# Optimization experiments

Hardware: AMD Instinct MI355X
Metric: run time of the kernel (lower is better)

Reference implementation:

```python
import jax, jax.numpy as jnp
import numpy as np

N = 100000   # nodes
E = 800000   # edges
H = 4        # heads
C = 32       # out_channels (== in_channels)
IN = 32      # in_channels
ED = 16      # edge_dim
RBF_IN = 42  # sbf_dim*6 (input to lin_rbf)
SBF_IN = 16  # rbf_dim (input to lin_sbf)


def _glorot(key, shape):
    fan_in = shape[0]
    return jax.random.normal(key, shape, dtype=jnp.float32) / np.sqrt(fan_in).astype(np.float32)


def setup_inputs() -> dict:
    key = jax.random.key(0)
    ks = jax.random.split(key, 20)
    inp = {
        "x": jax.random.normal(ks[0], (N, IN), dtype=jnp.float32),
        "edge_attr": jax.random.normal(ks[1], (E, ED), dtype=jnp.float32),
        "rbf": jax.random.normal(ks[2], (N, RBF_IN), dtype=jnp.float32),
        "sbf": jax.random.normal(ks[3], (E, H, SBF_IN), dtype=jnp.float32),
        # params (weights stored [in, out] for y = x @ W)
        "w_rbf0": _glorot(ks[4], (RBF_IN, IN)),
        "w_rbf1": _glorot(ks[5], (IN, IN)),
        "w_sbf0": _glorot(ks[6], (SBF_IN, IN)),
        "w_sbf1": _glorot(ks[7], (IN, IN)),
        "w_ek": _glorot(ks[8], (ED, H * C)),
        "w_ev": _glorot(ks[9], (ED, H * C)),
        "w_k": _glorot(ks[10], (IN, H * C)),
        "b_k": jnp.zeros((H * C,), dtype=jnp.float32),
        "w_q": _glorot(ks[11], (IN, H * C)),
        "b_q": jnp.zeros((H * C,), dtype=jnp.float32),
        "w_v": _glorot(ks[12], (IN, H * C)),
        "b_v": jnp.zeros((H * C,), dtype=jnp.float32),
        "w_skip": _glorot(ks[13], (IN, H * C)),
        "b_skip": jnp.zeros((H * C,), dtype=jnp.float32),
        "edge_index": jax.random.randint(ks[14], (2, E), 0, N, dtype=jnp.int32),
        "edge_index_0": jax.random.randint(ks[15], (E,), 0, N, dtype=jnp.int32),  # unused by forward
    }
    return inp


def reference(x, edge_attr, rbf, sbf,
              w_rbf0, w_rbf1, w_sbf0, w_sbf1,
              w_ek, w_ev, w_k, b_k, w_q, b_q, w_v, b_v,
              w_skip, b_skip, edge_index, edge_index_0):
    src, dst = edge_index[0], edge_index[1]
    # filters (source swaps rbf/sbf naming; we follow forward() exactly)
    rbf_filter = (rbf @ w_rbf0) @ w_rbf1            # [N, IN]
    sbf_filter = (sbf @ w_sbf0) @ w_sbf1            # [E, H, C]

    x_src = rbf_filter * x                          # [N, IN]
    key = (x_src @ w_k + b_k).reshape(-1, H, C)     # [N, H, C]
    query = (x @ w_q + b_q).reshape(-1, H, C)
    value = (x_src @ w_v + b_v).reshape(-1, H, C)

    edge_key = (edge_attr @ w_ek).reshape(-1, H, C)  # [E, H, C]
    edge_val = (edge_attr @ w_ev).reshape(-1, H, C)

    key_j = key[src] + edge_key                     # gather + add [E, H, C]
    value_j = value[src] + edge_val
    query_i = query[dst]

    inv_sqrt_c = np.float32(1.0 / np.sqrt(C))
    alpha = (query_i * key_j).sum(axis=-1) * inv_sqrt_c   # [E, H]

    # segment softmax over destination nodes
    amax = jax.ops.segment_max(alpha, dst, num_segments=N)
    amax = jnp.where(jnp.isfinite(amax), amax, 0.0)
    ex = jnp.exp(alpha - amax[dst])
    denom = jax.ops.segment_sum(ex, dst, num_segments=N)
    alpha = ex / (denom[dst] + np.float32(1e-16))         # [E, H]

    # dropout p=0.0 -> identity
    message = value_j * alpha[:, :, None] * sbf_filter    # [E, H, C]
    aggr = jax.ops.segment_sum(message, dst, num_segments=N)  # [N, H, C]

    out = aggr.reshape(N, H * C) + (x @ w_skip + b_skip)  # concat + root skip
    return out
```

## Files before the change

kernel.cpp:

```cpp
#include <hip/hip_runtime.h>
#include <hip/hip_bf16.h>

#define NN 100000
#define EE 800000
#define SLOT 64

typedef unsigned short u16;

__device__ __forceinline__ float bf2f(u16 u){ return __uint_as_float(((unsigned)u)<<16); }
__device__ __forceinline__ u16 f2bf(float f){
  unsigned u = __float_as_uint(f);
  u += 0x7fffu + ((u>>16)&1u);
  return (u16)(u>>16);
}
__device__ __forceinline__ float lo16(unsigned v){ return __uint_as_float(v<<16); }
__device__ __forceinline__ float hi16(unsigned v){ return __uint_as_float(v & 0xffff0000u); }

__device__ __forceinline__ void cvt8(uint4 u, float* f){
  f[0]=lo16(u.x); f[1]=hi16(u.x);
  f[2]=lo16(u.y); f[3]=hi16(u.y);
  f[4]=lo16(u.z); f[5]=hi16(u.z);
  f[6]=lo16(u.w); f[7]=hi16(u.w);
}

__global__ void kprep(const float* w_rbf0, const float* w_rbf1, const float* w_sbf0, const float* w_sbf1,
                      const float* w_k, const float* b_k, const float* w_q, const float* b_q,
                      const float* w_v, const float* b_v, const float* w_skip, const float* b_skip,
                      float* Wrbfc, float* Wsbfc,
                      float2* wkv, float2* wqs, float2* bkv, float2* bqs)
{
  int b = blockIdx.x;
  if (b==0){
    for (int idx=threadIdx.x; idx<42*32; idx+=blockDim.x){
      int k=idx>>5, c=idx&31;
      float acc=0.f;
      for (int j=0;j<32;j++) acc += w_rbf0[k*32+j]*w_rbf1[j*32+c];
      Wrbfc[idx]=acc;
    }
  } else if (b==1){
    for (int idx=threadIdx.x; idx<16*32; idx+=blockDim.x){
      int k=idx>>5, c=idx&31;
      float acc=0.f;
      for (int j=0;j<32;j++) acc += w_sbf0[k*32+j]*w_sbf1[j*32+c];
      Wsbfc[idx]=acc;
    }
  } else if (b==2){
    for (int idx=threadIdx.x; idx<4096; idx+=blockDim.x){
      wkv[idx]=make_float2(w_k[idx], w_v[idx]);
      wqs[idx]=make_float2(w_q[idx], w_skip[idx]);
    }
  } else {
    for (int idx=threadIdx.x; idx<128; idx+=blockDim.x){
      bkv[idx]=make_float2(b_k[idx], b_v[idx]);
      bqs[idx]=make_float2(b_q[idx], b_skip[idx]);
    }
  }
}

__global__ void kscatter(const int* ei, int* cnt, int* slots){
  int e = blockIdx.x*blockDim.x + threadIdx.x;
  if (e < EE){
    int dst = ei[EE+e];
    int pos = atomicAdd(&cnt[dst], 1);
    if (pos < SLOT) slots[(long)dst*SLOT+pos] = e;
  }
}

__global__ void __launch_bounds__(256) knode(const float* x, const float* rbf, const float* Wrbfc,
                                             const float2* wkv_g, const float2* wqs_g,
                                             const float2* bkv_g, const float2* bqs_g,
                                             u16* key, u16* value, u16* query, float* outp)
{
  __shared__ float2 wkv[4096];
  __shared__ float2 wqs[4096];
  __shared__ float  Wr[42*32];
  __shared__ float2 bkv[128], bqs[128];
  __shared__ float  xs[2][32], xsrcs[2][32], rbfs[2][42];
  for (int i=threadIdx.x;i<4096;i+=256){ wkv[i]=wkv_g[i]; wqs[i]=wqs_g[i]; }
  for (int i=threadIdx.x;i<1344;i+=256) Wr[i]=Wrbfc[i];
  if (threadIdx.x<128){ bkv[threadIdx.x]=bkv_g[threadIdx.x]; bqs[threadIdx.x]=bqs_g[threadIdx.x]; }
  __syncthreads();
  int half = threadIdx.x>>7, t = threadIdx.x&127;
  for (long p = blockIdx.x; p*2 < NN; p += gridDim.x){
    long n = p*2 + half;
    if (t<32)                xs[half][t]      = x[n*32+t];
    else if (t>=64 && t<106) rbfs[half][t-64] = rbf[n*42+(t-64)];
    __syncthreads();
    if (t<32){
      float acc=0.f;
      #pragma unroll
      for (int k=0;k<42;k++) acc += rbfs[half][k]*Wr[k*32+t];
      xsrcs[half][t] = acc*xs[half][t];
    }
    __syncthreads();
    {
      float2 b1 = bkv[t], b2 = bqs[t];
      float ak=b1.x, av=b1.y, aq=b2.x, as=b2.y;
      #pragma unroll
      for (int k=0;k<32;k++){
        float xv = xsrcs[half][k];
        float xq = xs[half][k];
        float2 w1 = wkv[(k<<7)+t];
        float2 w2 = wqs[(k<<7)+t];
        ak += xv*w1.x; av += xv*w1.y;
        aq += xq*w2.x; as += xq*w2.y;
      }
      key  [n*128+t] = f2bf(ak);
      value[n*128+t] = f2bf(av);
      query[n*128+t] = f2bf(aq);
      outp [n*128+t] = as;
    }
    __syncthreads();
  }
}

__global__ void __launch_bounds__(256) kalpha2(const float* edge_attr, const int* ei,
                                               const float* wek_g, const u16* key, const u16* query,
                                               float* alpha)
{
  __shared__ __align__(16) float wek[2048];
  __shared__ float eas[64][17];
  __shared__ int srcs[64], dsts[64];
  for (int idx=threadIdx.x; idx<2048; idx+=256) wek[idx]=wek_g[idx];
  int g = threadIdx.x>>4, l = threadIdx.x&15;
  int h = l>>2;
  for (long base=(long)blockIdx.x*64; base<EE; base+=(long)gridDim.x*64){
    __syncthreads();
    {
      const float4* s4 = (const float4*)(edge_attr + base*16);
      float4 v = s4[threadIdx.x];
      int e = threadIdx.x>>2, c0 = (threadIdx.x&3)<<2;
      eas[e][c0]=v.x; eas[e][c0+1]=v.y; eas[e][c0+2]=v.z; eas[e][c0+3]=v.w;
      if (threadIdx.x < 64)       srcs[threadIdx.x]    = ei[base + threadIdx.x];
      else if (threadIdx.x < 128) dsts[threadIdx.x-64] = ei[EE + base + threadIdx.x-64];
    }
    __syncthreads();
    float ek[4][8];
    #pragma unroll
    for (int j=0;j<4;j++){
      #pragma unroll
      for (int i=0;i<8;i++) ek[j][i]=0.f;
    }
    #pragma unroll
    for (int k=0;k<16;k++){
      const float4* w4 = (const float4*)&wek[(k<<7)+(l<<3)];
      float4 wa=w4[0], wb=w4[1];
      #pragma unroll
      for (int j=0;j<4;j++){
        float ea = eas[(g<<2)+j][k];
        ek[j][0]+=ea*wa.x; ek[j][1]+=ea*wa.y; ek[j][2]+=ea*wa.z; ek[j][3]+=ea*wa.w;
        ek[j][4]+=ea*wb.x; ek[j][5]+=ea*wb.y; ek[j][6]+=ea*wb.z; ek[j][7]+=ea*wb.w;
      }
    }
    #pragma unroll
    for (int j=0;j<4;j++){
      int el = (g<<2)+j;
      long e = base + el;
      int src = srcs[el], dst = dsts[el];
      float q8[8], k8[8];
      uint4 ku = *(const uint4*)(key   + (long)src*128 + l*8);
      uint4 qu = *(const uint4*)(query + (long)dst*128 + l*8);
      cvt8(ku,k8); cvt8(qu,q8);
      float part=0.f;
      #pragma unroll
      for (int i=0;i<8;i++) part += q8[i]*(k8[i]+ek[j][i]);
      part += __shfl_xor(part,1);
      part += __shfl_xor(part,2);
      if ((l&3)==0) alpha[e*4+h] = part*0.17677669529663687f;
    }
  }
}

__global__ void __launch_bounds__(256,4) kaggr_wave(const float* edge_attr, const float* sbf,
                                                    const int* ei, const float* wev_g, const float* Wsbfc,
                                                    const u16* value, const float* alpha,
                                                    const int* cnt, const int* slots, float* outp)
{
  __shared__ float4 wlds[4][SLOT];
  int wid = threadIdx.x>>6;
  int l   = threadIdx.x&63;
  int dst = blockIdx.x*4 + wid;
  int c = cnt[dst]; if (c > SLOT) c = SLOT;
  if (c == 0) return;
  int h = l>>4;

  float2 wv[16], ws[16];
  #pragma unroll
  for (int k=0;k<16;k++){
    wv[k] = *(const float2*)&wev_g[k*128 + 2*l];
    ws[k] = *(const float2*)&Wsbfc[k*32 + ((2*l)&31)];
  }

  const int* sl = slots + (long)dst*SLOT;
  int e_l = 0, src_l = 0;
  if (l < c){ e_l = sl[l]; src_l = ei[e_l]; }

  float4 araw = make_float4(-3.0e38f,-3.0e38f,-3.0e38f,-3.0e38f);
  if (l < c) araw = *(const float4*)(alpha + (long)e_l*4);

  int e0 = __shfl(e_l, 0), s0 = __shfl(src_l, 0);
  float    earN = edge_attr[(long)e0*16 + (l&15)];
  float    svN  = sbf[(long)e0*64 + l];
  unsigned vvN  = *(const unsigned*)(value + (long)s0*128 + 2*l);

  float4 m4 = araw;
  #pragma unroll
  for (int off=1; off<=32; off<<=1){
    m4.x = fmaxf(m4.x, __shfl_xor(m4.x, off));
    m4.y = fmaxf(m4.y, __shfl_xor(m4.y, off));
    m4.z = fmaxf(m4.z, __shfl_xor(m4.z, off));
    m4.w = fmaxf(m4.w, __shfl_xor(m4.w, off));
  }
  float4 ex4 = make_float4(0.f,0.f,0.f,0.f);
  if (l < c){
    ex4.x = __expf(araw.x - m4.x);
    ex4.y = __expf(araw.y - m4.y);
    ex4.z = __expf(araw.z - m4.z);
    ex4.w = __expf(araw.w - m4.w);
  }
  float4 d4 = ex4;
  #pragma unroll
  for (int off=1; off<=32; off<<=1){
    d4.x += __shfl_xor(d4.x, off);
    d4.y += __shfl_xor(d4.y, off);
    d4.z += __shfl_xor(d4.z, off);
    d4.w += __shfl_xor(d4.w, off);
  }
  if (l < c){
    float4 w4;
    w4.x = ex4.x / (d4.x + 1e-16f);
    w4.y = ex4.y / (d4.y + 1e-16f);
    w4.z = ex4.z / (d4.z + 1e-16f);
    w4.w = ex4.w / (d4.w + 1e-16f);
    wlds[wid][l] = w4;
  }

  float2 seed = *(const float2*)(outp + (long)dst*128 + 2*l);
  float acc0 = seed.x, acc1 = seed.y;

  for (int i=0;i<c;i++){
    float ear = earN; float sv = svN; unsigned vv = vvN;
    if (i+1 < c){
      int e1 = __shfl(e_l, i+1), s1 = __shfl(src_l, i+1);
      earN = edge_attr[(long)e1*16 + (l&15)];
      svN  = sbf[(long)e1*64 + l];
      vvN  = *(const unsigned*)(value + (long)s1*128 + 2*l);
    }
    float w = *((const float*)&wlds[wid][i] + h);
    float ev0=0.f, ev1=0.f, f0=0.f, f1=0.f;
    #pragma unroll
    for (int k=0;k<16;k++){
      float eak = __shfl(ear, k, 16);
      float sk  = __shfl(sv, (l & 48) + k);
      ev0 += eak*wv[k].x; ev1 += eak*wv[k].y;
      f0  += sk *ws[k].x; f1  += sk *ws[k].y;
    }
    float v0 = lo16(vv), v1 = hi16(vv);
    acc0 += (v0+ev0)*(w*f0);
    acc1 += (v1+ev1)*(w*f1);
  }

  *(float2*)(outp + (long)dst*128 + 2*l) = make_float2(acc0, acc1);
}

extern "C" void kernel_launch(void* const* d_in, const int* in_sizes, int n_in,
                              void* d_out, int out_size, void* d_ws, size_t ws_size,
                              hipStream_t stream)
{
  const float* x         = (const float*)d_in[0];
  const float* edge_attr = (const float*)d_in[1];
  const float* rbf       = (const float*)d_in[2];
  const float* sbf       = (const float*)d_in[3];
  const float* w_rbf0    = (const float*)d_in[4];
  const float* w_rbf1    = (const float*)d_in[5];
  const float* w_sbf0    = (const float*)d_in[6];
  const float* w_sbf1    = (const float*)d_in[7];
  const float* w_ek      = (const float*)d_in[8];
  const float* w_ev      = (const float*)d_in[9];
  const float* w_k       = (const float*)d_in[10];
  const float* b_k       = (const float*)d_in[11];
  const float* w_q       = (const float*)d_in[12];
  const float* b_q       = (const float*)d_in[13];
  const float* w_v       = (const float*)d_in[14];
  const float* b_v       = (const float*)d_in[15];
  const float* w_skip    = (const float*)d_in[16];
  const float* b_skip    = (const float*)d_in[17];
  const int* ei          = (const int*)d_in[18];
  float* out = (float*)d_out;

  char* ws = (char*)d_ws;
  u16*   key   = (u16*)  (ws + 0);
  u16*   query = (u16*)  (ws + 25600000);
  u16*   value = (u16*)  (ws + 51200000);
  float* alpha = (float*)(ws + 76800000);
  int*   slots = (int*)  (ws + 89600000);
  int*   cnt   = (int*)  (ws + 115200000);
  float* Wrbfc = (float*)(ws + 115600000);
  float* Wsbfc = (float*)(ws + 115608192);
  float2* wkv  = (float2*)(ws + 115612288);
  float2* wqs  = (float2*)(ws + 115645056);
  float2* bkv  = (float2*)(ws + 115677824);
  float2* bqs  = (float2*)(ws + 115678848);

  kprep<<<4,256,0,stream>>>(w_rbf0,w_rbf1,w_sbf0,w_sbf1,w_k,b_k,w_q,b_q,w_v,b_v,w_skip,b_skip,
                            Wrbfc,Wsbfc,wkv,wqs,bkv,bqs);
  hipMemsetAsync(cnt, 0, NN*sizeof(int), stream);
  kscatter<<<3125,256,0,stream>>>(ei, cnt, slots);
  knode<<<1024,256,0,stream>>>(x,rbf,Wrbfc,wkv,wqs,bkv,bqs,key,value,query,out);
  kalpha2<<<2500,256,0,stream>>>(edge_attr,ei,w_ek,key,query,alpha);
  kaggr_wave<<<25000,256,0,stream>>>(edge_attr,sbf,ei,w_ev,Wsbfc,value,alpha,cnt,slots,out);
}
```

Before: 1.049 ms.

## Precompute per-node query-projected edge-key weights to shrink per-edge alpha work

Reassociates the attention score so the edge-key projection is folded into a per-destination-node table G = W_ek^T q, computed once per node. The per-edge alpha kernel then needs only a 16-wide dot with edge_attr plus the q·k dot, without staging W_ek or doing a 16x128 matmul per edge. The cost is an extra kernel, a 25.6MB workspace buffer, and an extra per-edge gather of G. The new path only runs when the workspace is large enough; otherwise it falls back to the old kernel.

```diff
diff --git a/kernel.cpp b/kernel.cpp
--- a/kernel.cpp
+++ b/kernel.cpp
@@ -111,6 +111,51 @@
       outp [n*128+t] = as;
     }
     __syncthreads();
+  }
+}
+
+__global__ void __launch_bounds__(256) kgcalc(const u16* query, const float* w_ek, float* G)
+{
+  __shared__ float wekT[128][17];
+  __shared__ float qs[4][129];
+  for (int i=threadIdx.x; i<2048; i+=256){
+    int kk=i>>7, cc=i&127;
+    wekT[cc][kk] = w_ek[i];
+  }
+  int t = threadIdx.x, nl = t>>6, j = t&63, h = j>>4, k = j&15;
+  const unsigned* qsrc = (const unsigned*)query;
+  __syncthreads();
+  for (long p = blockIdx.x; p*4 < NN; p += gridDim.x){
+    unsigned qd = qsrc[p*256 + t];
+    __syncthreads();
+    qs[nl][2*j]   = lo16(qd);
+    qs[nl][2*j+1] = hi16(qd);
+    __syncthreads();
+    float acc = 0.f;
+    #pragma unroll
+    for (int c=0;c<32;c++) acc += qs[nl][h*32+c]*wekT[h*32+c][k];
+    G[p*256 + t] = acc;
+  }
+}
+
+__global__ void __launch_bounds__(256) kalpha3(const float* edge_attr, const int* ei, const float* G,
+                                               const u16* key, const u16* query, float* alpha)
+{
+  int g = threadIdx.x>>4, l = threadIdx.x&15, h = l>>2, s = l&3;
+  for (long base=(long)blockIdx.x*16; base<EE; base+=(long)gridDim.x*16){
+    long e = base + g;
+    int src = ei[e], dst = ei[EE+e];
+    uint4  ku  = *(const uint4*)(key   + (long)src*128 + l*8);
+    uint4  qu  = *(const uint4*)(query + (long)dst*128 + l*8);
+    float4 G4  = *(const float4*)(G + (long)dst*64 + h*16 + s*4);
+    float4 ea4 = *(const float4*)(edge_attr + e*16 + s*4);
+    float k8[8], q8[8]; cvt8(ku,k8); cvt8(qu,q8);
+    float part = ea4.x*G4.x + ea4.y*G4.y + ea4.z*G4.z + ea4.w*G4.w;
+    #pragma unroll
+    for (int i=0;i<8;i++) part += q8[i]*k8[i];
+    part += __shfl_xor(part,1);
+    part += __shfl_xor(part,2);
+    if (s==0) alpha[e*4+h] = part*0.17677669529663687f;
   }
 }
 
@@ -301,12 +346,19 @@
   float2* wqs  = (float2*)(ws + 115645056);
   float2* bkv  = (float2*)(ws + 115677824);
   float2* bqs  = (float2*)(ws + 115678848);
+  float* G     = (float*)(ws + 115680256);
+  const size_t G_END = 115680256UL + (size_t)NN*64*4;
 
   kprep<<<4,256,0,stream>>>(w_rbf0,w_rbf1,w_sbf0,w_sbf1,w_k,b_k,w_q,b_q,w_v,b_v,w_skip,b_skip,
                             Wrbfc,Wsbfc,wkv,wqs,bkv,bqs);
   hipMemsetAsync(cnt, 0, NN*sizeof(int), stream);
   kscatter<<<3125,256,0,stream>>>(ei, cnt, slots);
   knode<<<1024,256,0,stream>>>(x,rbf,Wrbfc,wkv,wqs,bkv,bqs,key,value,query,out);
-  kalpha2<<<2500,256,0,stream>>>(edge_attr,ei,w_ek,key,query,alpha);
+  if (ws_size >= G_END){
+    kgcalc<<<2048,256,0,stream>>>(query, w_ek, G);
+    kalpha3<<<6250,256,0,stream>>>(edge_attr, ei, G, key, query, alpha);
+  } else {
+    kalpha2<<<2500,256,0,stream>>>(edge_attr,ei,w_ek,key,query,alpha);
+  }
   kaggr_wave<<<25000,256,0,stream>>>(edge_attr,sbf,ei,w_ev,Wsbfc,value,alpha,cnt,slots,out);
 }
```

New measurement: 1.088 ms. 3.8% more time.
